# Kernel tuning notes

Hardware: AMD Instinct MI355X
Metric: run time of the kernel (lower is better)

Reference implementation:

```python
import jax, jax.numpy as jnp
import numpy as np

B, T, HID = 1, 2048, 2048
H, KVH, D = 32, 8, 64
G = H // KVH          # kv groups = 4
SCALE = 1.0 / np.sqrt(D)
NEG = -1e9


def _rotate_half(x):
    x1, x2 = x[..., : D // 2], x[..., D // 2 :]
    return jnp.concatenate((-x2, x1), axis=-1)


def setup_inputs() -> dict:
    key = jax.random.key(0)
    ks = jax.random.split(key, 8)
    hidden_states = jax.random.normal(ks[0], (B, T, HID), jnp.float32)
    # RoPE tables (faithful shapes; realistic values)
    pos = jnp.arange(T, dtype=jnp.float32)[:, None]
    inv = 1.0 / (10000.0 ** (jnp.arange(0, D, 2, dtype=jnp.float32) / D))
    ang = pos * inv[None, :]                      # [T, D/2]
    ang = jnp.concatenate([ang, ang], axis=-1)    # [T, D]
    cos = jnp.broadcast_to(jnp.cos(ang)[None], (B, T, D))
    sin = jnp.broadcast_to(jnp.sin(ang)[None], (B, T, D))
    # causal additive mask [B,1,T,T]
    causal = jnp.tril(jnp.ones((T, T), bool))
    attention_mask_4d = jnp.where(causal, 0.0, NEG).astype(jnp.float32)[None, None]
    s = 0.02
    Wq = jax.random.normal(ks[1], (H * D, HID), jnp.float32) * s
    Wk = jax.random.normal(ks[2], (KVH * D, HID), jnp.float32) * s
    Wv = jax.random.normal(ks[3], (KVH * D, HID), jnp.float32) * s
    Wo = jax.random.normal(ks[4], (HID, H * D), jnp.float32) * s
    return {"hidden_states": hidden_states, "cos": cos, "sin": sin,
            "attention_mask_4d": attention_mask_4d,
            "Wq": Wq, "Wk": Wk, "Wv": Wv, "Wo": Wo}


def reference(hidden_states, cos, sin, attention_mask_4d, Wq, Wk, Wv, Wo):
    x = hidden_states
    b, t, _ = x.shape
    # QKV projections (nn.Linear: x @ W.T), then [B, heads, T, D]
    q = (x @ Wq.T).reshape(b, t, H, D).transpose(0, 2, 1, 3)
    k = (x @ Wk.T).reshape(b, t, KVH, D).transpose(0, 2, 1, 3)
    v = (x @ Wv.T).reshape(b, t, KVH, D).transpose(0, 2, 1, 3)
    # rotary: cos/sin [B,T,D] -> broadcast over heads
    c = cos[:, None]; s = sin[:, None]
    q = q * c + _rotate_half(q) * s
    k = k * c + _rotate_half(k) * s
    # grouped-query attention with fp32 scores/softmax
    qg = q.reshape(b, KVH, G, t, D)
    scores = jnp.einsum('bkgtd,bksd->bkgts', qg.astype(jnp.float32),
                        k.astype(jnp.float32)) * SCALE
    m = attention_mask_4d[:, 0].astype(jnp.float32)  # [B,T,S]
    scores = scores + m[:, None, None, :, :]
    probs = jax.nn.softmax(scores, axis=-1)
    out = jnp.einsum('bkgts,bksd->bkgtd', probs.astype(v.dtype), v)
    out = out.astype(q.dtype).reshape(b, H, t, D)
    out = out.transpose(0, 2, 1, 3).reshape(b, t, H * D)
    return out @ Wo.T
```

## Files before the change

### kernel.cpp

```cpp
#include <hip/hip_runtime.h>
#include <math.h>

typedef __attribute__((ext_vector_type(8))) __bf16 bf16x8;
typedef __attribute__((ext_vector_type(4))) float  f32x4;
typedef unsigned short ushort_t;
typedef unsigned int   uint_t;

static __device__ inline f32x4 mfma16(bf16x8 a, bf16x8 b, f32x4 c) {
    return __builtin_amdgcn_mfma_f32_16x16x32_bf16(a, b, c, 0, 0, 0);
}

static __device__ inline ushort_t f2b(float f) {
    uint_t u = __builtin_bit_cast(uint_t, f);
    u = (u + 0x7FFFu + ((u >> 16) & 1u)) >> 16;
    return (ushort_t)u;
}
static __device__ inline float b2f(ushort_t u) {
    uint_t x = ((uint_t)u) << 16;
    return __builtin_bit_cast(float, x);
}
static __device__ inline bf16x8 ld8(const ushort_t* p) {
    uint4 v = *(const uint4*)p;
    return __builtin_bit_cast(bf16x8, v);
}
static __device__ inline float fexp2(float x) {
#if __has_builtin(__builtin_amdgcn_exp2f)
    return __builtin_amdgcn_exp2f(x);
#else
    return exp2f(x);
#endif
}

static __device__ inline void gl_lds16(const ushort_t* g, ushort_t* l) {
    __builtin_amdgcn_global_load_lds(
        (const __attribute__((address_space(1))) void*)(g),
        (__attribute__((address_space(3))) void*)(l),
        16, 0, 0);
}

#define WS_XB     0
#define WS_WQKV   8388608
#define WS_WO     20971520
#define WS_P0     29360128
#define WS_P1     41943040
#define WS_QBB    0
#define WS_KBB    8388608
#define WS_VTG    10485760
#define WS_AB     12582912
#define WS_O0     29360128
#define WS_O1     46137344

__global__ __launch_bounds__(256) void cvt_all(const float* __restrict__ x,
                                               const float* __restrict__ wq,
                                               const float* __restrict__ wk,
                                               const float* __restrict__ wv,
                                               const float* __restrict__ wo,
                                               ushort_t* __restrict__ dst) {
    const size_t i = (size_t)(blockIdx.x * 256 + threadIdx.x) * 4;
    const float* src; size_t off;
    if (i < 4194304)       { src = x;  off = 0; }
    else if (i < 8388608)  { src = wq; off = 4194304; }
    else if (i < 9437184)  { src = wk; off = 8388608; }
    else if (i < 10485760) { src = wv; off = 9437184; }
    else                   { src = wo; off = 10485760; }
    float4 v = *(const float4*)(src + (i - off));
    ushort4 o;
    o.x = f2b(v.x); o.y = f2b(v.y); o.z = f2b(v.z); o.w = f2b(v.w);
    *(ushort4*)(dst + i) = o;
}

template <int OUTB>
static __device__ void gemm_tile(const ushort_t* __restrict__ A,
                                 const ushort_t* __restrict__ Bt,
                                 void* __restrict__ Cout,
                                 int N, int K, long m0, long n0,
                                 int kbeg, int kend,
                                 ushort_t* As, ushort_t* Bs) {
    const int tid  = threadIdx.x;
    const int lane = tid & 63, wave = tid >> 6;
    const int wr = wave >> 1, wc = wave & 1;
    const int qn = lane & 15, quad = lane >> 4;

    const ushort_t* ga = A  + (m0 + lane) * K + wave * 8;
    const ushort_t* gb = Bt + (n0 + lane) * K + wave * 8;
    ushort_t* laL = As + wave * 1024;
    ushort_t* laH = As + (wave + 4) * 1024;
    ushort_t* lbL = Bs + wave * 1024;
    ushort_t* lbH = Bs + (wave + 4) * 1024;

    f32x4 zero = {0.f, 0.f, 0.f, 0.f};
    f32x4 acc[4][4];
    for (int i = 0; i < 4; i++)
        for (int j = 0; j < 4; j++) acc[i][j] = zero;

    const long r64 = 64L * K;
    for (int k0 = kbeg; k0 < kend; k0 += 64) {
        __syncthreads();
        gl_lds16(ga + k0,            laL);
        gl_lds16(ga + r64 + k0,      laL + 512);
        gl_lds16(ga + k0 + 32,       laH);
        gl_lds16(ga + r64 + k0 + 32, laH + 512);
        gl_lds16(gb + k0,            lbL);
        gl_lds16(gb + r64 + k0,      lbL + 512);
        gl_lds16(gb + k0 + 32,       lbH);
        gl_lds16(gb + r64 + k0 + 32, lbH + 512);
        __syncthreads();
        #pragma unroll
        for (int kk = 0; kk < 2; kk++) {
            bf16x8 af[4], bfr[4];
            const int cb = (kk * 4 + quad) * 1024;
            #pragma unroll
            for (int i = 0; i < 4; i++)
                af[i] = *(const bf16x8*)(As + cb + (wr * 64 + i * 16 + qn) * 8);
            #pragma unroll
            for (int j = 0; j < 4; j++)
                bfr[j] = *(const bf16x8*)(Bs + cb + (wc * 64 + j * 16 + qn) * 8);
            #pragma unroll
            for (int i = 0; i < 4; i++)
                #pragma unroll
                for (int j = 0; j < 4; j++)
                    acc[i][j] = mfma16(af[i], bfr[j], acc[i][j]);
        }
    }
    #pragma unroll
    for (int i = 0; i < 4; i++)
        #pragma unroll
        for (int j = 0; j < 4; j++)
            #pragma unroll
            for (int r = 0; r < 4; r++) {
                long row = m0 + wr * 64 + i * 16 + quad * 4 + r;
                long col = n0 + wc * 64 + j * 16 + qn;
                if (OUTB)
                    ((ushort_t*)Cout)[row * N + col] = f2b(acc[i][j][r]);
                else
                    ((float*)Cout)[row * N + col] = acc[i][j][r];
            }
}

template <int OUTB>
__global__ __launch_bounds__(256) void gemm_split(const ushort_t* __restrict__ A,
                                                  const ushort_t* __restrict__ Bt,
                                                  void* __restrict__ C0,
                                                  void* __restrict__ C1,
                                                  int N, int K) {
    __shared__ ushort_t As[8192];
    __shared__ ushort_t Bs[8192];
    const int half = blockIdx.z;
    const int kh = K >> 1;
    gemm_tile<OUTB>(A, Bt, half ? C1 : C0, N, K,
                    (long)blockIdx.y * 128, (long)blockIdx.x * 128,
                    half * kh, half * kh + kh, As, Bs);
}

__global__ __launch_bounds__(256) void fuse_crv(const ushort_t* __restrict__ p0,
                                                const ushort_t* __restrict__ p1,
                                                const float* __restrict__ cs,
                                                const float* __restrict__ sn,
                                                ushort_t* __restrict__ qd,
                                                ushort_t* __restrict__ kd,
                                                ushort_t* __restrict__ vt) {
    __shared__ ushort_t tl[64][65];
    const int cx = blockIdx.x;
    const int ty = blockIdx.y;
    const int r  = threadIdx.x >> 2;
    const int c0 = (threadIdx.x & 3) << 4;
    const int t  = ty * 64 + r;
    const size_t base = (size_t)t * 3072 + cx * 64;

    if (cx < 40) {
        const int cp = c0 ^ 32;
        float own[16], par[16];
        #pragma unroll
        for (int jj = 0; jj < 2; jj++) {
            uint4 a = *(const uint4*)(p0 + base + c0 + jj * 8);
            uint4 b = *(const uint4*)(p1 + base + c0 + jj * 8);
            uint4 c = *(const uint4*)(p0 + base + cp + jj * 8);
            uint4 d = *(const uint4*)(p1 + base + cp + jj * 8);
            const ushort_t* pa = (const ushort_t*)&a;
            const ushort_t* pb = (const ushort_t*)&b;
            const ushort_t* pc = (const ushort_t*)&c;
            const ushort_t* pd = (const ushort_t*)&d;
            #pragma unroll
            for (int e = 0; e < 8; e++) {
                own[jj * 8 + e] = b2f(pa[e]) + b2f(pb[e]);
                par[jj * 8 + e] = b2f(pc[e]) + b2f(pd[e]);
            }
        }
        float cs16[16], sn16[16];
        #pragma unroll
        for (int jj = 0; jj < 4; jj++) {
            float4 c4 = *(const float4*)(cs + (size_t)t * 64 + c0 + jj * 4);
            float4 s4 = *(const float4*)(sn + (size_t)t * 64 + c0 + jj * 4);
            cs16[jj * 4 + 0] = c4.x; cs16[jj * 4 + 1] = c4.y;
            cs16[jj * 4 + 2] = c4.z; cs16[jj * 4 + 3] = c4.w;
            sn16[jj * 4 + 0] = s4.x; sn16[jj * 4 + 1] = s4.y;
            sn16[jj * 4 + 2] = s4.z; sn16[jj * 4 + 3] = s4.w;
        }
        const float scale = (cx < 32) ? 0.18033688f : 1.0f;
        union { ushort_t u[16]; uint4 v[2]; } o;
        #pragma unroll
        for (int j = 0; j < 16; j++) {
            const int d = c0 + j;
            const float pr = (d < 32) ? -par[j] : par[j];
            o.u[j] = f2b((own[j] * cs16[j] + pr * sn16[j]) * scale);
        }
        if (cx < 32) {
            ushort_t* dst = qd + (size_t)t * 2048 + cx * 64 + c0;
            *(uint4*)dst = o.v[0]; *(uint4*)(dst + 8) = o.v[1];
        } else {
            ushort_t* dst = kd + (size_t)t * 512 + (cx - 32) * 64 + c0;
            *(uint4*)dst = o.v[0]; *(uint4*)(dst + 8) = o.v[1];
        }
    } else {
        #pragma unroll
        for (int jj = 0; jj < 2; jj++) {
            uint4 a = *(const uint4*)(p0 + base + c0 + jj * 8);
            uint4 b = *(const uint4*)(p1 + base + c0 + jj * 8);
            const ushort_t* pa = (const ushort_t*)&a;
            const ushort_t* pb = (const ushort_t*)&b;
            #pragma unroll
            for (int e = 0; e < 8; e++)
                tl[r][c0 + jj * 8 + e] = f2b(b2f(pa[e]) + b2f(pb[e]));
        }
        __syncthreads();
        const int rr  = threadIdx.x >> 3;
        const int cc8 = (threadIdx.x & 7) * 8;
        const int db = (cx - 40) * 64, tb = ty * 64;
        #pragma unroll
        for (int h = 0; h < 2; h++) {
            const int d = rr + h * 32;
            ushort4 o0, o1;
            o0.x = tl[cc8 + 0][d]; o0.y = tl[cc8 + 1][d];
            o0.z = tl[cc8 + 2][d]; o0.w = tl[cc8 + 3][d];
            o1.x = tl[cc8 + 4][d]; o1.y = tl[cc8 + 5][d];
            o1.z = tl[cc8 + 6][d]; o1.w = tl[cc8 + 7][d];
            *(ushort4*)(vt + (size_t)(db + d) * 2048 + tb + cc8)     = o0;
            *(ushort4*)(vt + (size_t)(db + d) * 2048 + tb + cc8 + 4) = o1;
        }
    }
}

__global__ __launch_bounds__(256) void combine_o(const float4* __restrict__ s0,
                                                 const float4* __restrict__ s1,
                                                 float4* __restrict__ out) {
    for (int i = blockIdx.x * 256 + threadIdx.x; i < 1048576; i += 2048 * 256) {
        float4 a = s0[i], b = s1[i];
        float4 r; r.x = a.x + b.x; r.y = a.y + b.y; r.z = a.z + b.z; r.w = a.w + b.w;
        out[i] = r;
    }
}

__global__ __launch_bounds__(256) void attn_kernel(const ushort_t* __restrict__ Q,
                                                   const ushort_t* __restrict__ Kb,
                                                   const ushort_t* __restrict__ Vt,
                                                   ushort_t* __restrict__ Ob) {
    __shared__ ushort_t Ks[2 * 4096];
    __shared__ ushort_t Vs[2 * 4096];
    __shared__ ushort_t pl[4 * 32 * 72];
    const int tid  = threadIdx.x;
    const int lane = tid & 63, wid = tid >> 6;
    const int qn = lane & 15, quad = lane >> 4;
    const int h   = blockIdx.x & 31;
    const int qb  = 15 - (blockIdx.x >> 5);
    const int kvb = (h >> 2) * 64;
    const int trow = qb * 128 + wid * 32;
    ushort_t* plw = pl + wid * 32 * 72;
    f32x4 zero = {0.f, 0.f, 0.f, 0.f};

    const ushort_t* qpA = Q + (size_t)(trow + qn) * 2048 + h * 64 + quad * 8;
    const bf16x8 qA0 = ld8(qpA), qA1 = ld8(qpA + 32);
    const ushort_t* qpB = qpA + 16 * 2048;
    const bf16x8 qB0 = ld8(qpB), qB1 = ld8(qpB + 32);

    f32x4 oA[4] = {zero, zero, zero, zero};
    f32x4 oB[4] = {zero, zero, zero, zero};
    float lA[4] = {0.f, 0.f, 0.f, 0.f};
    float lB[4] = {0.f, 0.f, 0.f, 0.f};
    const int ntiles = qb * 2 + 2;

#define STAGE(s0, buf)                                                         \
    do {                                                                       \
        const ushort_t* kg = Kb + (size_t)((s0) + lane) * 512 + kvb + wid * 8; \
        gl_lds16(kg,      Ks + (buf) * 4096 + wid * 512);                      \
        gl_lds16(kg + 32, Ks + (buf) * 4096 + (wid + 4) * 512);                \
        const ushort_t* vg = Vt + (size_t)(kvb + lane) * 2048 + (s0) + wid * 8;\
        gl_lds16(vg,      Vs + (buf) * 4096 + wid * 512);                      \
        gl_lds16(vg + 32, Vs + (buf) * 4096 + (wid + 4) * 512);                \
    } while (0)

#define COMPUTE(s0, buf)                                                       \
    do {                                                                       \
        f32x4 scA[4], scB[4];                                                  \
        _Pragma("unroll")                                                      \
        for (int cb = 0; cb < 4; cb++) {                                       \
            const bf16x8 kf0 = *(const bf16x8*)(Ks + (buf) * 4096 + quad * 512 + (cb * 16 + qn) * 8);       \
            const bf16x8 kf1 = *(const bf16x8*)(Ks + (buf) * 4096 + (quad + 4) * 512 + (cb * 16 + qn) * 8); \
            f32x4 s = mfma16(qA0, kf0, zero); scA[cb] = mfma16(qA1, kf1, s);   \
            f32x4 t = mfma16(qB0, kf0, zero); scB[cb] = mfma16(qB1, kf1, t);   \
        }                                                                      \
        const bool needmask = ((s0) + 63 > trow);                              \
        _Pragma("unroll")                                                      \
        for (int i = 0; i < 4; i++) {                                          \
            const int tA = trow + quad * 4 + i, tB = tA + 16;                  \
            _Pragma("unroll")                                                  \
            for (int cb = 0; cb < 4; cb++) {                                   \
                const int col = (s0) + cb * 16 + qn;                           \
                float vA = scA[cb][i], vB = scB[cb][i];                        \
                if (needmask) {                                                \
                    if (col > tA) vA = -INFINITY;                              \
                    if (col > tB) vB = -INFINITY;                              \
                }                                                              \
                const float pA = fexp2(vA), pB = fexp2(vB);                    \
                lA[i] += pA; lB[i] += pB;                                      \
                plw[(quad * 4 + i) * 72 + cb * 16 + qn]      = f2b(pA);        \
                plw[(16 + quad * 4 + i) * 72 + cb * 16 + qn] = f2b(pB);        \
            }                                                                  \
        }                                                                      \
        const bf16x8 pfA0 = *(const bf16x8*)(plw + qn * 72 + quad * 8);        \
        const bf16x8 pfA1 = *(const bf16x8*)(plw + qn * 72 + 32 + quad * 8);   \
        const bf16x8 pfB0 = *(const bf16x8*)(plw + (16 + qn) * 72 + quad * 8); \
        const bf16x8 pfB1 = *(const bf16x8*)(plw + (16 + qn) * 72 + 32 + quad * 8); \
        _Pragma("unroll")                                                      \
        for (int dcb = 0; dcb < 4; dcb++) {                                    \
            const bf16x8 vf0 = *(const bf16x8*)(Vs + (buf) * 4096 + quad * 512 + (dcb * 16 + qn) * 8);       \
            const bf16x8 vf1 = *(const bf16x8*)(Vs + (buf) * 4096 + (quad + 4) * 512 + (dcb * 16 + qn) * 8); \
            oA[dcb] = mfma16(pfA0, vf0, oA[dcb]);                              \
            oA[dcb] = mfma16(pfA1, vf1, oA[dcb]);                              \
            oB[dcb] = mfma16(pfB0, vf0, oB[dcb]);                              \
            oB[dcb] = mfma16(pfB1, vf1, oB[dcb]);                              \
        }                                                                      \
    } while (0)

    STAGE(0, 0);
    for (int t = 0; t < ntiles; t += 2) {
        __syncthreads();
        STAGE((t + 1) * 64, 1);
        COMPUTE(t * 64, 0);
        __syncthreads();
        if (t + 2 < ntiles) STAGE((t + 2) * 64, 0);
        COMPUTE((t + 1) * 64, 1);
    }
#undef STAGE
#undef COMPUTE

    #pragma unroll
    for (int i = 0; i < 4; i++) {
        float sA = lA[i], sB = lB[i];
        #pragma unroll
        for (int off = 1; off < 16; off <<= 1) {
            sA += __shfl_xor(sA, off, 64);
            sB += __shfl_xor(sB, off, 64);
        }
        const float invA = 1.0f / sA, invB = 1.0f / sB;
        ushort_t* obA = Ob + (size_t)(trow + quad * 4 + i) * 2048 + h * 64 + qn;
        ushort_t* obB = obA + 16 * 2048;
        obA[0]  = f2b(oA[0][i] * invA);
        obA[16] = f2b(oA[1][i] * invA);
        obA[32] = f2b(oA[2][i] * invA);
        obA[48] = f2b(oA[3][i] * invA);
        obB[0]  = f2b(oB[0][i] * invB);
        obB[16] = f2b(oB[1][i] * invB);
        obB[32] = f2b(oB[2][i] * invB);
        obB[48] = f2b(oB[3][i] * invB);
    }
}

extern "C" void kernel_launch(void* const* d_in, const int* in_sizes, int n_in,
                              void* d_out, int out_size, void* d_ws, size_t ws_size,
                              hipStream_t stream) {
    const float* x    = (const float*)d_in[0];
    const float* cosp = (const float*)d_in[1];
    const float* sinp = (const float*)d_in[2];
    const float* Wq = (const float*)d_in[4];
    const float* Wk = (const float*)d_in[5];
    const float* Wv = (const float*)d_in[6];
    const float* Wo = (const float*)d_in[7];
    char* ws = (char*)d_ws;
    (void)ws_size; (void)in_sizes; (void)n_in; (void)out_size;

    ushort_t* xb    = (ushort_t*)(ws + WS_XB);
    ushort_t* wqkvb = (ushort_t*)(ws + WS_WQKV);
    ushort_t* wob   = (ushort_t*)(ws + WS_WO);
    ushort_t* p0    = (ushort_t*)(ws + WS_P0);
    ushort_t* p1    = (ushort_t*)(ws + WS_P1);
    ushort_t* qbb   = (ushort_t*)(ws + WS_QBB);
    ushort_t* kbb   = (ushort_t*)(ws + WS_KBB);
    ushort_t* vtg   = (ushort_t*)(ws + WS_VTG);
    ushort_t* ab    = (ushort_t*)(ws + WS_AB);
    float*    o0    = (float*)   (ws + WS_O0);
    float*    o1    = (float*)   (ws + WS_O1);

    cvt_all<<<14336, 256, 0, stream>>>(x, Wq, Wk, Wv, Wo, xb);

    gemm_split<1><<<dim3(24, 16, 2), 256, 0, stream>>>(xb, wqkvb, p0, p1, 3072, 2048);

    fuse_crv<<<dim3(48, 32), 256, 0, stream>>>(p0, p1, cosp, sinp, qbb, kbb, vtg);

    attn_kernel<<<512, 256, 0, stream>>>(qbb, kbb, vtg, ab);

    gemm_split<0><<<dim3(16, 16, 2), 256, 0, stream>>>(ab, wob, o0, o1, 2048, 2048);

    combine_o<<<2048, 256, 0, stream>>>((const float4*)o0, (const float4*)o1,
                                        (float4*)d_out);
}
```

Before: 287.9 us.

## Halve attention query tile per block to double grid size

The attention kernel now gives each wave 16 query rows instead of 32, so a block covers 64 rows and the grid doubles to 1024 blocks. The main loop gains a tail step for an odd tile count, and the probability scratch buffer is resized with a row stride of 80. The aim is better occupancy and load balance across CUs under the causal triangle. In exchange, every K/V tile is loaded into LDS by twice as many blocks and each tile does fewer MFMAs, which lowers data reuse.

```diff
diff --git a/kernel.cpp b/kernel.cpp
--- a/kernel.cpp
+++ b/kernel.cpp
@@ -256,27 +256,23 @@
                                                    ushort_t* __restrict__ Ob) {
     __shared__ ushort_t Ks[2 * 4096];
     __shared__ ushort_t Vs[2 * 4096];
-    __shared__ ushort_t pl[4 * 32 * 72];
+    __shared__ ushort_t pl[4 * 16 * 80];
     const int tid  = threadIdx.x;
     const int lane = tid & 63, wid = tid >> 6;
     const int qn = lane & 15, quad = lane >> 4;
     const int h   = blockIdx.x & 31;
-    const int qb  = 15 - (blockIdx.x >> 5);
+    const int qb  = 31 - (blockIdx.x >> 5);
     const int kvb = (h >> 2) * 64;
-    const int trow = qb * 128 + wid * 32;
-    ushort_t* plw = pl + wid * 32 * 72;
+    const int trow = qb * 64 + wid * 16;
+    ushort_t* plw = pl + wid * 16 * 80;
     f32x4 zero = {0.f, 0.f, 0.f, 0.f};
 
     const ushort_t* qpA = Q + (size_t)(trow + qn) * 2048 + h * 64 + quad * 8;
     const bf16x8 qA0 = ld8(qpA), qA1 = ld8(qpA + 32);
-    const ushort_t* qpB = qpA + 16 * 2048;
-    const bf16x8 qB0 = ld8(qpB), qB1 = ld8(qpB + 32);
 
     f32x4 oA[4] = {zero, zero, zero, zero};
-    f32x4 oB[4] = {zero, zero, zero, zero};
     float lA[4] = {0.f, 0.f, 0.f, 0.f};
-    float lB[4] = {0.f, 0.f, 0.f, 0.f};
-    const int ntiles = qb * 2 + 2;
+    const int ntiles = qb + 1;
 
 #define STAGE(s0, buf)                                                         \
     do {                                                                       \
@@ -290,49 +286,43 @@
 
 #define COMPUTE(s0, buf)                                                       \
     do {                                                                       \
-        f32x4 scA[4], scB[4];                                                  \
+        f32x4 scA[4];                                                          \
         _Pragma("unroll")                                                      \
         for (int cb = 0; cb < 4; cb++) {                                       \
             const bf16x8 kf0 = *(const bf16x8*)(Ks + (buf) * 4096 + quad * 512 + (cb * 16 + qn) * 8);       \
             const bf16x8 kf1 = *(const bf16x8*)(Ks + (buf) * 4096 + (quad + 4) * 512 + (cb * 16 + qn) * 8); \
             f32x4 s = mfma16(qA0, kf0, zero); scA[cb] = mfma16(qA1, kf1, s);   \
-            f32x4 t = mfma16(qB0, kf0, zero); scB[cb] = mfma16(qB1, kf1, t);   \
         }                                                                      \
         const bool needmask = ((s0) + 63 > trow);                              \
         _Pragma("unroll")                                                      \
         for (int i = 0; i < 4; i++) {                                          \
-            const int tA = trow + quad * 4 + i, tB = tA + 16;                  \
+            const int tA = trow + quad * 4 + i;                                \
             _Pragma("unroll")                                                  \
             for (int cb = 0; cb < 4; cb++) {                                   \
                 const int col = (s0) + cb * 16 + qn;                           \
-                float vA = scA[cb][i], vB = scB[cb][i];                        \
+                float vA = scA[cb][i];                                         \
                 if (needmask) {                                                \
                     if (col > tA) vA = -INFINITY;                              \
-                    if (col > tB) vB = -INFINITY;                              \
                 }                                                              \
-                const float pA = fexp2(vA), pB = fexp2(vB);                    \
-                lA[i] += pA; lB[i] += pB;                                      \
-                plw[(quad * 4 + i) * 72 + cb * 16 + qn]      = f2b(pA);        \
-                plw[(16 + quad * 4 + i) * 72 + cb * 16 + qn] = f2b(pB);        \
+                const float pA = fexp2(vA);                                    \
+                lA[i] += pA;                                                   \
+                plw[(quad * 4 + i) * 80 + cb * 16 + qn] = f2b(pA);             \
             }                                                                  \
         }                                                                      \
-        const bf16x8 pfA0 = *(const bf16x8*)(plw + qn * 72 + quad * 8);        \
-        const bf16x8 pfA1 = *(const bf16x8*)(plw + qn * 72 + 32 + quad * 8);   \
-        const bf16x8 pfB0 = *(const bf16x8*)(plw + (16 + qn) * 72 + quad * 8); \
-        const bf16x8 pfB1 = *(const bf16x8*)(plw + (16 + qn) * 72 + 32 + quad * 8); \
+        const bf16x8 pfA0 = *(const bf16x8*)(plw + qn * 80 + quad * 8);        \
+        const bf16x8 pfA1 = *(const bf16x8*)(plw + qn * 80 + 32 + quad * 8);   \
         _Pragma("unroll")                                                      \
         for (int dcb = 0; dcb < 4; dcb++) {                                    \
             const bf16x8 vf0 = *(const bf16x8*)(Vs + (buf) * 4096 + quad * 512 + (dcb * 16 + qn) * 8);       \
             const bf16x8 vf1 = *(const bf16x8*)(Vs + (buf) * 4096 + (quad + 4) * 512 + (dcb * 16 + qn) * 8); \
             oA[dcb] = mfma16(pfA0, vf0, oA[dcb]);                              \
             oA[dcb] = mfma16(pfA1, vf1, oA[dcb]);                              \
-            oB[dcb] = mfma16(pfB0, vf0, oB[dcb]);                              \
-            oB[dcb] = mfma16(pfB1, vf1, oB[dcb]);                              \
         }                                                                      \
     } while (0)
 
     STAGE(0, 0);
-    for (int t = 0; t < ntiles; t += 2) {
+    int t = 0;
+    for (; t + 2 <= ntiles; t += 2) {
         __syncthreads();
         STAGE((t + 1) * 64, 1);
         COMPUTE(t * 64, 0);
@@ -340,28 +330,25 @@
         if (t + 2 < ntiles) STAGE((t + 2) * 64, 0);
         COMPUTE((t + 1) * 64, 1);
     }
+    if (t < ntiles) {
+        __syncthreads();
+        COMPUTE(t * 64, 0);
+    }
 #undef STAGE
 #undef COMPUTE
 
     #pragma unroll
     for (int i = 0; i < 4; i++) {
-        float sA = lA[i], sB = lB[i];
-        #pragma unroll
-        for (int off = 1; off < 16; off <<= 1) {
+        float sA = lA[i];
+        #pragma unroll
+        for (int off = 1; off < 16; off <<= 1)
             sA += __shfl_xor(sA, off, 64);
-            sB += __shfl_xor(sB, off, 64);
-        }
-        const float invA = 1.0f / sA, invB = 1.0f / sB;
+        const float invA = 1.0f / sA;
         ushort_t* obA = Ob + (size_t)(trow + quad * 4 + i) * 2048 + h * 64 + qn;
-        ushort_t* obB = obA + 16 * 2048;
         obA[0]  = f2b(oA[0][i] * invA);
         obA[16] = f2b(oA[1][i] * invA);
         obA[32] = f2b(oA[2][i] * invA);
         obA[48] = f2b(oA[3][i] * invA);
-        obB[0]  = f2b(oB[0][i] * invB);
-        obB[16] = f2b(oB[1][i] * invB);
-        obB[32] = f2b(oB[2][i] * invB);
-        obB[48] = f2b(oB[3][i] * invB);
     }
 }
 
@@ -396,7 +383,7 @@
 
     fuse_crv<<<dim3(48, 32), 256, 0, stream>>>(p0, p1, cosp, sinp, qbb, kbb, vtg);
 
-    attn_kernel<<<512, 256, 0, stream>>>(qbb, kbb, vtg, ab);
+    attn_kernel<<<1024, 256, 0, stream>>>(qbb, kbb, vtg, ab);
 
     gemm_split<0><<<dim3(16, 16, 2), 256, 0, stream>>>(ab, wob, o0, o1, 2048, 2048);
 
```

New measurement: 278.2 us. -3.4%, faster.
